# Kernel optimization log

Hardware: AMD Instinct MI355X
Metric: run time of the kernel (lower is better)

The kernel has to match this reference:

```python
import jax, jax.numpy as jnp
import numpy as np

HEADS, DIM_HEAD, C, B, HS, WS = 8, 64, 512, 2, 48, 48


def setup_inputs() -> dict:
    key = jax.random.key(0)
    ks = jax.random.split(key, 9)
    s = 0.02
    return {
        "hidden_states": jax.random.normal(ks[0], (B, C, HS, WS), jnp.float32),
        "Wq": jax.random.normal(ks[1], (HEADS, DIM_HEAD, C), jnp.float32) * s,
        "bq": jax.random.normal(ks[2], (HEADS, DIM_HEAD), jnp.float32) * s,
        "Wk": jax.random.normal(ks[3], (HEADS, DIM_HEAD, C), jnp.float32) * s,
        "bk": jax.random.normal(ks[4], (HEADS, DIM_HEAD), jnp.float32) * s,
        "Wv": jax.random.normal(ks[5], (HEADS, DIM_HEAD, C), jnp.float32) * s,
        "bv": jax.random.normal(ks[6], (HEADS, DIM_HEAD), jnp.float32) * s,
        "Wo": jax.random.normal(ks[7], (C, HEADS * DIM_HEAD), jnp.float32) * s,
        "bo": jax.random.normal(ks[8], (C,), jnp.float32) * s,
    }


def reference(hidden_states, Wq, bq, Wk, bk, Wv, bv, Wo, bo):
    # hidden_states: [B, C, H, W]; per-head 1x1 convs == per-head linear over C.
    b, c, h, w = hidden_states.shape
    hw = h * w
    x = hidden_states.reshape(b, c, hw)  # [B, C, HW]
    # Batched per-head projections (fuses the per-head Conv2d loop).
    q = jnp.einsum('bcs,ndc->bnsd', x, Wq) + bq[None, :, None, :]  # [B, n, HW, d]
    k = jnp.einsum('bcs,ndc->bnsd', x, Wk) + bk[None, :, None, :]
    v = jnp.einsum('bcs,ndc->bnsd', x, Wv) + bv[None, :, None, :]
    scale = 1.0 / jnp.sqrt(jnp.asarray(DIM_HEAD, hidden_states.dtype))
    scores = jnp.einsum('bnqd,bnkd->bnqk', q, k) * scale  # [B, n, HW, HW]
    probs = jax.nn.softmax(scores, axis=-1)
    attn = jnp.einsum('bnqk,bnkd->bnqd', probs, v)  # [B, n, HW, d]
    # concat heads along last dim (matches torch.cat(..., dim=-1))
    attn = attn.transpose(0, 2, 1, 3).reshape(b, hw, HEADS * DIM_HEAD)
    out = attn @ Wo.T + bo  # [B, HW, C] (to_out[0]; to_out[1] dropout = identity)
    out = out.reshape(b, h, w, c).transpose(0, 3, 1, 2)  # [B, C, H, W]
    return out
```

## Files before the change

kernel.cpp:

```cpp
#include <hip/hip_runtime.h>
#include <hip/hip_bf16.h>

#define HEADS 8
#define DHEAD 64
#define CDIM  512
#define SEQ   2304
#define ND    512
#define NCHUNK 4

typedef unsigned short u16;
typedef unsigned int   u32;
typedef __attribute__((ext_vector_type(8))) short short8;
typedef __attribute__((ext_vector_type(4))) float f32x4;

#define QSCALE 0.18033688011112043f

__device__ __forceinline__ u16 f2bf(float f) {
    union { float f; u32 u; } x; x.f = f;
    u32 r = x.u + 0x7FFFu + ((x.u >> 16) & 1u);
    return (u16)(r >> 16);
}
__device__ __forceinline__ float bf2f(u16 v) {
    union { u32 u; float f; } x; x.u = ((u32)v) << 16; return x.f;
}
__device__ __forceinline__ u32 pkbf(float a, float b) {
    union { float f; u32 u; } x, y; x.f = a; y.f = b;
    return __builtin_amdgcn_perm(y.u + 0x8000u, x.u + 0x8000u, 0x07060302u);
}
__device__ __forceinline__ f32x4 mfma16(short8 a, short8 b, f32x4 c) {
    return __builtin_amdgcn_mfma_f32_16x16x32_bf16(a, b, c, 0, 0, 0);
}
__device__ __forceinline__ void cp16(const void* g, void* l) {
    __builtin_amdgcn_global_load_lds(
        (const __attribute__((address_space(1))) u32*)(uintptr_t)g,
        (__attribute__((address_space(3))) u32*)(u32)(uintptr_t)l,
        16, 0, 0);
}
__device__ __forceinline__ int kperm_inv(int r) {
    return (r & ~0x1C) | ((r & 0x0C) << 1) | ((r & 0x10) >> 2);
}

__global__ void prep_kernel(const float* __restrict__ H,
                            const float* __restrict__ Wq, const float* __restrict__ Wk,
                            const float* __restrict__ Wv, const float* __restrict__ Wo,
                            u16* __restrict__ Wqkv, u16* __restrict__ Wob,
                            u16* __restrict__ X) {
    __shared__ float tile[32][33];
    const int t = threadIdx.x;
    const int bx = blockIdx.x;
    if (bx < 1024) {
        const int N1 = CDIM * ND;
        int i4 = (bx * 256 + t) * 4;
        float4 v;
        if (i4 < N1)             v = *(const float4*)&Wq[i4];
        else if (i4 < 2 * N1)    v = *(const float4*)&Wk[i4 - N1];
        else if (i4 < 3 * N1)    v = *(const float4*)&Wv[i4 - 2 * N1];
        else                     v = *(const float4*)&Wo[i4 - 3 * N1];
        uint2 o;
        o.x = pkbf(v.x, v.y);
        o.y = pkbf(v.z, v.w);
        u16* d = (i4 < 3 * N1) ? &Wqkv[i4] : &Wob[i4 - 3 * N1];
        *(uint2*)d = o;
    } else {
        int bb = bx - 1024;
        int st = bb % 72, ct = (bb / 72) % 16, b = bb / (72 * 16);
        int tx = t & 31, ty = t >> 5;
#pragma unroll
        for (int k = 0; k < 4; ++k) {
            int c = ct * 32 + ty + k * 8;
            tile[ty + k * 8][tx] = H[((size_t)b * CDIM + c) * SEQ + st * 32 + tx];
        }
        __syncthreads();
#pragma unroll
        for (int k = 0; k < 4; ++k) {
            int s = st * 32 + ty + k * 8;
            X[((size_t)b * SEQ + s) * CDIM + ct * 32 + tx] = f2bf(tile[tx][ty + k * 8]);
        }
    }
}

__global__ __launch_bounds__(256) void gemm_qkv_kernel(
        const u16* __restrict__ W, const u16* __restrict__ X,
        const float* __restrict__ bq, const float* __restrict__ bk, const float* __restrict__ bv,
        u16* __restrict__ Q, u16* __restrict__ K, u16* __restrict__ V) {
    __shared__ __align__(16) u16 sm[2 * (64 * 64 + 128 * 64)];
    const int n0 = blockIdx.x * 128;
    const int m0 = blockIdx.y * 64;
    const int b  = blockIdx.z;
    const int t = threadIdx.x;
    const int lane = t & 63, w = t >> 6;
    const int l16 = lane & 15, quad = lane >> 4;
    const int x7 = l16 & 7;
    const int srow = t >> 3, scol = (t & 7) * 8;
    const int scol_sw = ((t & 7) ^ (srow & 7)) * 8;
    const u16* Xb = X + (size_t)b * SEQ * CDIM;

    f32x4 acc[4][2] = {};

    {
        u16* As = sm; u16* Bs = sm + 4096;
#pragma unroll
        for (int it = 0; it < 2; ++it) {
            int r2 = it * 32 + srow;
            cp16(&W[(size_t)(m0 + r2) * 512 + scol_sw], &As[r2 * 64 + scol]);
        }
#pragma unroll
        for (int it = 0; it < 4; ++it) {
            int r2 = it * 32 + srow;
            cp16(&Xb[(size_t)(n0 + r2) * 512 + scol_sw], &Bs[r2 * 64 + scol]);
        }
    }
    for (int kb = 0; kb < 512; kb += 64) {
        const int pb = (kb >> 6) & 1;
        const u16* As = sm + pb * 12288;
        const u16* Bs = As + 4096;
        __syncthreads();
        if (kb + 64 < 512) {
            u16* An = sm + (pb ^ 1) * 12288;
            u16* Bn = An + 4096;
#pragma unroll
            for (int it = 0; it < 2; ++it) {
                int r2 = it * 32 + srow;
                cp16(&W[(size_t)(m0 + r2) * 512 + kb + 64 + scol_sw], &An[r2 * 64 + scol]);
            }
#pragma unroll
            for (int it = 0; it < 4; ++it) {
                int r2 = it * 32 + srow;
                cp16(&Xb[(size_t)(n0 + r2) * 512 + kb + 64 + scol_sw], &Bn[r2 * 64 + scol]);
            }
        }
#pragma unroll
        for (int kk = 0; kk < 2; ++kk) {
            const int co = ((kk * 4 + quad) ^ x7) * 8;
            short8 af[4], bfr[2];
#pragma unroll
            for (int i = 0; i < 4; ++i)
                af[i] = *(const short8*)&As[(i * 16 + l16) * 64 + co];
#pragma unroll
            for (int j = 0; j < 2; ++j)
                bfr[j] = *(const short8*)&Bs[(w * 32 + j * 16 + l16) * 64 + co];
#pragma unroll
            for (int i = 0; i < 4; ++i)
#pragma unroll
                for (int j = 0; j < 2; ++j)
                    acc[i][j] = mfma16(af[i], bfr[j], acc[i][j]);
        }
    }

    if (m0 < 1024) {
        const bool isQ = (m0 < 512);
        const float* bias = isQ ? bq : bk;
        const float sc = isQ ? QSCALE : 1.0f;
        const int mq = isQ ? m0 : m0 - 512;
        u16* dst = isQ ? Q : K;
#pragma unroll
        for (int j = 0; j < 2; ++j) {
            int s = n0 + w * 32 + j * 16 + l16;
#pragma unroll
            for (int i = 0; i < 4; ++i) {
                int mm = mq + i * 16 + quad * 4;
                uint2 val;
                val.x = pkbf((acc[i][j][0] + bias[mm + 0]) * sc, (acc[i][j][1] + bias[mm + 1]) * sc);
                val.y = pkbf((acc[i][j][2] + bias[mm + 2]) * sc, (acc[i][j][3] + bias[mm + 3]) * sc);
                *(uint2*)&dst[(((size_t)(b * 8 + (mm >> 6))) * SEQ + s) * 64 + (mm & 63)] = val;
            }
        }
    } else {
#pragma unroll
        for (int j = 0; j < 2; ++j) {
            int s = n0 + w * 32 + j * 16 + l16;
#pragma unroll
            for (int i = 0; i < 4; ++i) {
                int mbase = m0 - 1024 + i * 16 + quad * 4;
#pragma unroll
                for (int r = 0; r < 4; ++r) {
                    int mm = mbase + r;
                    V[((size_t)(b * 512 + mm)) * SEQ + s] = f2bf(acc[i][j][r] + bv[mm]);
                }
            }
        }
    }
}

__global__ __launch_bounds__(256, 3) void attn_partial(
        const u16* __restrict__ Q,
        const u16* __restrict__ K,
        const u16* __restrict__ Vt,
        u16* __restrict__ Opart,
        float* __restrict__ Lpart) {
    __shared__ __align__(16) u16 sm[2 * 8192];
    const int pair = blockIdx.x & 15, qt = blockIdx.x >> 4;
    const int c = blockIdx.y;
    const int b = pair >> 3, h = pair & 7;
    const int t = threadIdx.x, lane = t & 63, w = t >> 6;
    const int l16 = lane & 15, quad = lane >> 4;
    const int x7 = l16 & 7;
    const int srow = t >> 3;
    const int scol = (t & 7) * 8;
    const int scol_sw = ((t & 7) ^ (srow & 7)) * 8;
    const int kinv0 = kperm_inv(srow), kinv1 = kperm_inv(32 + srow);
    const int cA = (quad ^ x7) * 8;
    const int cB = (quad ^ x7 ^ 4) * 8;

    const u16* Qg = Q + ((size_t)pair * SEQ + qt * 192) * 64;
    const int rA = w * 16 + l16;
    short8 qf[3][2];
#pragma unroll
    for (int G = 0; G < 3; ++G) {
        qf[G][0] = *(const short8*)&Qg[(size_t)(G * 64 + rA) * 64 + quad * 8];
        qf[G][1] = *(const short8*)&Qg[(size_t)(G * 64 + rA) * 64 + 32 + quad * 8];
    }

    const u16* Kg = K  + ((size_t)pair * SEQ + c * 576) * 64;
    const u16* Vg = Vt + ((size_t)(b * 512 + h * 64)) * SEQ + c * 576;

    float lacc[3] = {0.f, 0.f, 0.f};
    f32x4 o[3][4] = {};

    {
        u16* Ks = sm; u16* Vs = sm + 4096;
        cp16(&Kg[(size_t)kinv0 * 64 + scol_sw], &Ks[srow * 64 + scol]);
        cp16(&Kg[(size_t)kinv1 * 64 + scol_sw], &Ks[(32 + srow) * 64 + scol]);
        cp16(&Vg[(size_t)srow * SEQ + scol_sw],        &Vs[srow * 64 + scol]);
        cp16(&Vg[(size_t)(32 + srow) * SEQ + scol_sw], &Vs[(32 + srow) * 64 + scol]);
    }
    for (int kt = 0; kt < 9; ++kt) {
        const int pb = kt & 1;
        const u16* Ks = sm + pb * 8192;
        const u16* Vs = Ks + 4096;
        __syncthreads();
        if (kt < 8) {
            u16* Kn = sm + (pb ^ 1) * 8192;
            u16* Vn = Kn + 4096;
            cp16(&Kg[(size_t)((kt + 1) * 64 + kinv0) * 64 + scol_sw], &Kn[srow * 64 + scol]);
            cp16(&Kg[(size_t)((kt + 1) * 64 + kinv1) * 64 + scol_sw], &Kn[(32 + srow) * 64 + scol]);
            cp16(&Vg[(size_t)srow * SEQ + (kt + 1) * 64 + scol_sw],        &Vn[srow * 64 + scol]);
            cp16(&Vg[(size_t)(32 + srow) * SEQ + (kt + 1) * 64 + scol_sw], &Vn[(32 + srow) * 64 + scol]);
        }
        f32x4 sacc[3][4];
#pragma unroll
        for (int j = 0; j < 4; ++j) {
            short8 kf0 = *(const short8*)&Ks[(j * 16 + l16) * 64 + cA];
            short8 kf1 = *(const short8*)&Ks[(j * 16 + l16) * 64 + cB];
#pragma unroll
            for (int G = 0; G < 3; ++G) {
                f32x4 z = {0.f, 0.f, 0.f, 0.f};
                z = mfma16(kf0, qf[G][0], z);
                sacc[G][j] = mfma16(kf1, qf[G][1], z);
            }
        }
        u32 pk[3][8];
#pragma unroll
        for (int G = 0; G < 3; ++G)
#pragma unroll
            for (int j = 0; j < 4; ++j) {
                float e0 = __builtin_amdgcn_exp2f(sacc[G][j][0]);
                float e1 = __builtin_amdgcn_exp2f(sacc[G][j][1]);
                float e2 = __builtin_amdgcn_exp2f(sacc[G][j][2]);
                float e3 = __builtin_amdgcn_exp2f(sacc[G][j][3]);
                lacc[G] += (e0 + e1) + (e2 + e3);
                pk[G][2 * j]     = pkbf(e0, e1);
                pk[G][2 * j + 1] = pkbf(e2, e3);
            }
#pragma unroll
        for (int g = 0; g < 2; ++g) {
            const int cg = g ? cB : cA;
#pragma unroll
            for (int i = 0; i < 4; ++i) {
                short8 vf = *(const short8*)&Vs[(i * 16 + l16) * 64 + cg];
#pragma unroll
                for (int G = 0; G < 3; ++G) {
                    short8 pf;
                    u32* pw = (u32*)&pf;
                    pw[0] = pk[G][4 * g + 0];
                    pw[1] = pk[G][4 * g + 1];
                    pw[2] = pk[G][4 * g + 2];
                    pw[3] = pk[G][4 * g + 3];
                    o[G][i] = mfma16(vf, pf, o[G][i]);
                }
            }
        }
    }
    float linv[3];
#pragma unroll
    for (int G = 0; G < 3; ++G) {
        float lr = lacc[G];
        lr += __shfl_xor(lr, 16);
        lr += __shfl_xor(lr, 32);
        if (quad == 0) Lpart[((size_t)(c * 16 + pair)) * SEQ + qt * 192 + G * 64 + rA] = lr;
        linv[G] = 1.0f / lr;
    }
    const size_t orow = ((size_t)(c * 16 + pair)) * SEQ + qt * 192;

    __syncthreads();
#pragma unroll
    for (int G = 0; G < 3; ++G)
#pragma unroll
        for (int i = 0; i < 4; ++i) {
            uint2 pkv;
            pkv.x = pkbf(o[G][i][0] * linv[G], o[G][i][1] * linv[G]);
            pkv.y = pkbf(o[G][i][2] * linv[G], o[G][i][3] * linv[G]);
            *(uint2*)&sm[(G * 64 + rA) * 72 + i * 16 + quad * 4] = pkv;
        }
    __syncthreads();
#pragma unroll
    for (int it = 0; it < 6; ++it) {
        int v = it * 256 + t;
        int row = v >> 3, col = (v & 7) * 8;
        *(uint4*)&Opart[(orow + row) * 64 + col] = *(const uint4*)&sm[row * 72 + col];
    }
}

__global__ __launch_bounds__(256) void attn_combine(
        const u16* __restrict__ Opart, const float* __restrict__ Lpart,
        u16* __restrict__ At) {
    const int bid = blockIdx.x;
    const int pair = bid / 144, sb = bid % 144;
    const int tid = threadIdx.x;
    const int rl = tid >> 4, dg = tid & 15;
    const int s = sb * 16 + rl;
    const int b = pair >> 3, h = pair & 7;
    float wc[NCHUNK], L = 0.f;
#pragma unroll
    for (int c = 0; c < NCHUNK; ++c) {
        wc[c] = Lpart[(size_t)(c * 16 + pair) * SEQ + s];
        L += wc[c];
    }
    float invL = 1.0f / L;
    float acc[4] = {0.f, 0.f, 0.f, 0.f};
#pragma unroll
    for (int c = 0; c < NCHUNK; ++c) {
        ushort4 v = *(const ushort4*)&Opart[((size_t)(c * 16 + pair) * SEQ + s) * 64 + dg * 4];
        acc[0] += wc[c] * bf2f(v.x);
        acc[1] += wc[c] * bf2f(v.y);
        acc[2] += wc[c] * bf2f(v.z);
        acc[3] += wc[c] * bf2f(v.w);
    }
    uint2 outv;
    outv.x = pkbf(acc[0] * invL, acc[1] * invL);
    outv.y = pkbf(acc[2] * invL, acc[3] * invL);
    *(uint2*)&At[((size_t)b * SEQ + s) * ND + h * 64 + dg * 4] = outv;
}

__global__ __launch_bounds__(256) void gemm_out_kernel(
        const u16* __restrict__ Wob, const u16* __restrict__ At,
        const float* __restrict__ bo, float* __restrict__ out) {
    __shared__ __align__(16) u16 sm[2 * 8192];
    const int n0 = blockIdx.x * 64;
    const int m0 = blockIdx.y * 64;
    const int b  = blockIdx.z;
    const int t = threadIdx.x;
    const int lane = t & 63, w = t >> 6;
    const int l16 = lane & 15, quad = lane >> 4;
    const int x7 = l16 & 7;
    const int srow = t >> 3, scol = (t & 7) * 8;
    const int scol_sw = ((t & 7) ^ (srow & 7)) * 8;
    const u16* Ab = At + (size_t)b * SEQ * ND;

    f32x4 acc[4] = {};

    {
        u16* As = sm; u16* Bs = sm + 4096;
#pragma unroll
        for (int it = 0; it < 2; ++it) {
            int r2 = it * 32 + srow;
            cp16(&Wob[(size_t)(m0 + r2) * 512 + scol_sw], &As[r2 * 64 + scol]);
            cp16(&Ab [(size_t)(n0 + r2) * 512 + scol_sw], &Bs[r2 * 64 + scol]);
        }
    }
    for (int kb = 0; kb < 512; kb += 64) {
        const int pb = (kb >> 6) & 1;
        const u16* As = sm + pb * 8192;
        const u16* Bs = As + 4096;
        __syncthreads();
        if (kb + 64 < 512) {
            u16* An = sm + (pb ^ 1) * 8192;
            u16* Bn = An + 4096;
#pragma unroll
            for (int it = 0; it < 2; ++it) {
                int r2 = it * 32 + srow;
                cp16(&Wob[(size_t)(m0 + r2) * 512 + kb + 64 + scol_sw], &An[r2 * 64 + scol]);
                cp16(&Ab [(size_t)(n0 + r2) * 512 + kb + 64 + scol_sw], &Bn[r2 * 64 + scol]);
            }
        }
#pragma unroll
        for (int kk = 0; kk < 2; ++kk) {
            const int co = ((kk * 4 + quad) ^ x7) * 8;
            short8 af[4];
#pragma unroll
            for (int i = 0; i < 4; ++i)
                af[i] = *(const short8*)&As[(i * 16 + l16) * 64 + co];
            short8 bfr = *(const short8*)&Bs[(w * 16 + l16) * 64 + co];
#pragma unroll
            for (int i = 0; i < 4; ++i)
                acc[i] = mfma16(af[i], bfr, acc[i]);
        }
    }
#pragma unroll
    for (int i = 0; i < 4; ++i) {
        int cbase = m0 + i * 16 + quad * 4;
        int s = n0 + w * 16 + l16;
#pragma unroll
        for (int r = 0; r < 4; ++r) {
            int cc = cbase + r;
            __builtin_nontemporal_store(acc[i][r] + bo[cc],
                                        &out[((size_t)(b * 512 + cc)) * SEQ + s]);
        }
    }
}

extern "C" void kernel_launch(void* const* d_in, const int* in_sizes, int n_in,
                              void* d_out, int out_size, void* d_ws, size_t ws_size,
                              hipStream_t stream) {
    const float* H  = (const float*)d_in[0];
    const float* Wq = (const float*)d_in[1];
    const float* bq = (const float*)d_in[2];
    const float* Wk = (const float*)d_in[3];
    const float* bk = (const float*)d_in[4];
    const float* Wv = (const float*)d_in[5];
    const float* bv = (const float*)d_in[6];
    const float* Wo = (const float*)d_in[7];
    const float* bo = (const float*)d_in[8];
    float* out = (float*)d_out;

    u16* ws    = (u16*)d_ws;
    u16* Wqkv  = ws;
    u16* Wob   = Wqkv  + 1536 * 512;
    u16* Xbf   = Wob   + 512 * 512;
    u16* Qb    = Xbf   + 2 * SEQ * CDIM;
    u16* Kb    = Qb    + 2 * SEQ * ND;
    u16* Vb    = Kb    + 2 * SEQ * ND;
    u16* At    = Vb    + 2 * SEQ * ND;
    u16* Opart = At    + 2 * SEQ * ND;
    float* Lpart = (float*)(Opart + NCHUNK * 16 * SEQ * 64);

    prep_kernel<<<3328, 256, 0, stream>>>(H, Wq, Wk, Wv, Wo, Wqkv, Wob, Xbf);
    gemm_qkv_kernel<<<dim3(18, 24, 2), 256, 0, stream>>>(Wqkv, Xbf, bq, bk, bv, Qb, Kb, Vb);
    attn_partial<<<dim3(192, NCHUNK), 256, 0, stream>>>(Qb, Kb, Vb, Opart, Lpart);
    attn_combine<<<2304, 256, 0, stream>>>(Opart, Lpart, At);
    gemm_out_kernel<<<dim3(36, 8, 2), 256, 0, stream>>>(Wob, At, bo, out);
}
```

Before: 134.2 us.

## Stage V transpose via LDS, use hardware bf16 pack, setprio, widen combine

Several unrelated changes land together. The V epilogue of the QKV GEMM now stages its tile in shared memory and writes 16-byte coalesced rows instead of scattered 2-byte stores. The attention kernel uses v_cvt_pk_bf16_f32 for packing, keeps P fragments as short8 vectors, and raises wave priority around the MFMA sections. The combine kernel processes 8 elements per thread with 16-byte loads and stores on half as many blocks. The hardware convert may round differently from the manual rounding, and the V staging relies on the LDS tile being large enough and free after the main loop.

After: 129.8 us. 3.3% less time.

```diff
diff --git a/kernel.cpp b/kernel.cpp
--- a/kernel.cpp
+++ b/kernel.cpp
@@ -26,6 +26,11 @@
 __device__ __forceinline__ u32 pkbf(float a, float b) {
     union { float f; u32 u; } x, y; x.f = a; y.f = b;
     return __builtin_amdgcn_perm(y.u + 0x8000u, x.u + 0x8000u, 0x07060302u);
+}
+__device__ __forceinline__ u32 cvtpk(float lo, float hi) {
+    u32 r;
+    asm("v_cvt_pk_bf16_f32 %0, %1, %2" : "=v"(r) : "v"(lo), "v"(hi));
+    return r;
 }
 __device__ __forceinline__ f32x4 mfma16(short8 a, short8 b, f32x4 c) {
     return __builtin_amdgcn_mfma_f32_16x16x32_bf16(a, b, c, 0, 0, 0);
@@ -166,18 +171,27 @@
             }
         }
     } else {
+        __syncthreads();
+        u16* vb = sm;
+        const int mv = m0 - 1024;
 #pragma unroll
         for (int j = 0; j < 2; ++j) {
-            int s = n0 + w * 32 + j * 16 + l16;
+            int sl = w * 32 + j * 16 + l16;
 #pragma unroll
             for (int i = 0; i < 4; ++i) {
-                int mbase = m0 - 1024 + i * 16 + quad * 4;
-#pragma unroll
-                for (int r = 0; r < 4; ++r) {
-                    int mm = mbase + r;
-                    V[((size_t)(b * 512 + mm)) * SEQ + s] = f2bf(acc[i][j][r] + bv[mm]);
-                }
-            }
+                int mb = i * 16 + quad * 4;
+#pragma unroll
+                for (int r = 0; r < 4; ++r)
+                    vb[(mb + r) * 144 + sl] = f2bf(acc[i][j][r] + bv[mv + mb + r]);
+            }
+        }
+        __syncthreads();
+#pragma unroll
+        for (int k2 = 0; k2 < 4; ++k2) {
+            int v = k2 * 256 + t;
+            int row = v >> 4, ch = (v & 15) * 8;
+            *(uint4*)&V[((size_t)(b * 512 + mv + row)) * SEQ + n0 + ch] =
+                *(const uint4*)&vb[row * 144 + ch];
         }
     }
 }
@@ -238,6 +252,7 @@
             cp16(&Vg[(size_t)(32 + srow) * SEQ + (kt + 1) * 64 + scol_sw], &Vn[(32 + srow) * 64 + scol]);
         }
         f32x4 sacc[3][4];
+        __builtin_amdgcn_s_setprio(1);
 #pragma unroll
         for (int j = 0; j < 4; ++j) {
             short8 kf0 = *(const short8*)&Ks[(j * 16 + l16) * 64 + cA];
@@ -249,7 +264,8 @@
                 sacc[G][j] = mfma16(kf1, qf[G][1], z);
             }
         }
-        u32 pk[3][8];
+        __builtin_amdgcn_s_setprio(0);
+        short8 pks[3][2];
 #pragma unroll
         for (int G = 0; G < 3; ++G)
 #pragma unroll
@@ -259,9 +275,11 @@
                 float e2 = __builtin_amdgcn_exp2f(sacc[G][j][2]);
                 float e3 = __builtin_amdgcn_exp2f(sacc[G][j][3]);
                 lacc[G] += (e0 + e1) + (e2 + e3);
-                pk[G][2 * j]     = pkbf(e0, e1);
-                pk[G][2 * j + 1] = pkbf(e2, e3);
-            }
+                u32* pw = (u32*)&pks[G][j >> 1];
+                pw[(j & 1) * 2 + 0] = cvtpk(e0, e1);
+                pw[(j & 1) * 2 + 1] = cvtpk(e2, e3);
+            }
+        __builtin_amdgcn_s_setprio(1);
 #pragma unroll
         for (int g = 0; g < 2; ++g) {
             const int cg = g ? cB : cA;
@@ -269,17 +287,11 @@
             for (int i = 0; i < 4; ++i) {
                 short8 vf = *(const short8*)&Vs[(i * 16 + l16) * 64 + cg];
 #pragma unroll
-                for (int G = 0; G < 3; ++G) {
-                    short8 pf;
-                    u32* pw = (u32*)&pf;
-                    pw[0] = pk[G][4 * g + 0];
-                    pw[1] = pk[G][4 * g + 1];
-                    pw[2] = pk[G][4 * g + 2];
-                    pw[3] = pk[G][4 * g + 3];
-                    o[G][i] = mfma16(vf, pf, o[G][i]);
-                }
-            }
-        }
+                for (int G = 0; G < 3; ++G)
+                    o[G][i] = mfma16(vf, pks[G][g], o[G][i]);
+            }
+        }
+        __builtin_amdgcn_s_setprio(0);
     }
     float linv[3];
 #pragma unroll
@@ -298,8 +310,8 @@
 #pragma unroll
         for (int i = 0; i < 4; ++i) {
             uint2 pkv;
-            pkv.x = pkbf(o[G][i][0] * linv[G], o[G][i][1] * linv[G]);
-            pkv.y = pkbf(o[G][i][2] * linv[G], o[G][i][3] * linv[G]);
+            pkv.x = cvtpk(o[G][i][0] * linv[G], o[G][i][1] * linv[G]);
+            pkv.y = cvtpk(o[G][i][2] * linv[G], o[G][i][3] * linv[G]);
             *(uint2*)&sm[(G * 64 + rA) * 72 + i * 16 + quad * 4] = pkv;
         }
     __syncthreads();
@@ -315,10 +327,10 @@
         const u16* __restrict__ Opart, const float* __restrict__ Lpart,
         u16* __restrict__ At) {
     const int bid = blockIdx.x;
-    const int pair = bid / 144, sb = bid % 144;
-    const int tid = threadIdx.x;
-    const int rl = tid >> 4, dg = tid & 15;
-    const int s = sb * 16 + rl;
+    const int pair = bid / 72, sb = bid % 72;
+    const int t = threadIdx.x;
+    const int rl = t >> 3, dg = t & 7;
+    const int s = sb * 32 + rl;
     const int b = pair >> 3, h = pair & 7;
     float wc[NCHUNK], L = 0.f;
 #pragma unroll
@@ -327,19 +339,21 @@
         L += wc[c];
     }
     float invL = 1.0f / L;
-    float acc[4] = {0.f, 0.f, 0.f, 0.f};
+    float acc[8] = {};
 #pragma unroll
     for (int c = 0; c < NCHUNK; ++c) {
-        ushort4 v = *(const ushort4*)&Opart[((size_t)(c * 16 + pair) * SEQ + s) * 64 + dg * 4];
-        acc[0] += wc[c] * bf2f(v.x);
-        acc[1] += wc[c] * bf2f(v.y);
-        acc[2] += wc[c] * bf2f(v.z);
-        acc[3] += wc[c] * bf2f(v.w);
-    }
-    uint2 outv;
+        uint4 v = *(const uint4*)&Opart[((size_t)(c * 16 + pair) * SEQ + s) * 64 + dg * 8];
+        const u16* pv = (const u16*)&v;
+#pragma unroll
+        for (int e = 0; e < 8; ++e)
+            acc[e] += wc[c] * bf2f(pv[e]);
+    }
+    uint4 outv;
     outv.x = pkbf(acc[0] * invL, acc[1] * invL);
     outv.y = pkbf(acc[2] * invL, acc[3] * invL);
-    *(uint2*)&At[((size_t)b * SEQ + s) * ND + h * 64 + dg * 4] = outv;
+    outv.z = pkbf(acc[4] * invL, acc[5] * invL);
+    outv.w = pkbf(acc[6] * invL, acc[7] * invL);
+    *(uint4*)&At[((size_t)b * SEQ + s) * ND + h * 64 + dg * 8] = outv;
 }
 
 __global__ __launch_bounds__(256) void gemm_out_kernel(
@@ -437,6 +451,6 @@
     prep_kernel<<<3328, 256, 0, stream>>>(H, Wq, Wk, Wv, Wo, Wqkv, Wob, Xbf);
     gemm_qkv_kernel<<<dim3(18, 24, 2), 256, 0, stream>>>(Wqkv, Xbf, bq, bk, bv, Qb, Kb, Vb);
     attn_partial<<<dim3(192, NCHUNK), 256, 0, stream>>>(Qb, Kb, Vb, Opart, Lpart);
-    attn_combine<<<2304, 256, 0, stream>>>(Opart, Lpart, At);
+    attn_combine<<<1152, 256, 0, stream>>>(Opart, Lpart, At);
     gemm_out_kernel<<<dim3(36, 8, 2), 256, 0, stream>>>(Wob, At, bo, out);
 }
```
